# Kernel tuning notes

Measured on AMD Instinct MI355X. Metric: run time of the kernel, lower is better.

Reference implementation:

```python
import jax, jax.numpy as jnp
import numpy as np

B, M, N, HID, H, P = 16, 1024, 1024, 512, 8, 2
DH = HID // H


def setup_inputs() -> dict:
    key = jax.random.key(0)
    k1, k2, k3, k4 = jax.random.split(key, 4)
    X = jax.random.normal(k1, (B, M, HID), dtype=jnp.float32)
    Y = jax.random.normal(k2, (B, N, HID), dtype=jnp.float32)
    # learned pad prefixes (kaiming-uniform in torch; any init is fine for a numerics baseline)
    bound = np.sqrt(1.0 / HID)
    pad_x = jax.random.uniform(k3, (P, HID), dtype=jnp.float32, minval=-bound, maxval=bound)
    pad_y = jax.random.uniform(k4, (P, HID), dtype=jnp.float32, minval=-bound, maxval=bound)
    return {"X": X, "Y": Y, "pad_x": pad_x, "pad_y": pad_y}


def _project(T, pad):
    # prepend learned pad rows, split into heads -> [B, H, L+P, DH]
    b = T.shape[0]
    T = jnp.concatenate([jnp.broadcast_to(pad[None], (b, P, HID)), T], axis=1)
    return T.reshape(b, T.shape[1], H, DH).transpose(0, 2, 1, 3)


def reference(X, Y, pad_x, pad_y):
    Xp = _project(X, pad_x)  # [B,H,Mp,DH], query=key=value
    Yp = _project(Y, pad_y)  # [B,H,Np,DH]
    # shared similarity matrix (no 1/sqrt(d) scaling in the original)
    sim = jnp.einsum('bhmd,bhnd->bhmn', Xp, Yp)  # [B,H,Mp,Np]
    # masks in the original are all-ones (pad rows + torch.ones), so masked_fill is a no-op
    attn_X_by_Y = jax.nn.softmax(sim, axis=2)  # softmax over Mp (rows)
    attn_Y_by_X = jax.nn.softmax(sim, axis=3)  # softmax over Np (cols)
    # X attends in Y: attn^T @ X_value -> [B,H,Np,DH]
    X_in_Y = jnp.einsum('bhmn,bhmd->bhnd', attn_X_by_Y, Xp)[:, :, P:, :]
    X_in_Y = X_in_Y.transpose(0, 2, 1, 3).reshape(X.shape[0], -1, HID)  # [B,N,HID]
    # Y attends in X: attn @ Y_value -> [B,H,Mp,DH]
    Y_in_X = jnp.einsum('bhmn,bhnd->bhmd', attn_Y_by_X, Yp)[:, :, P:, :]
    Y_in_X = Y_in_X.transpose(0, 2, 1, 3).reshape(Y.shape[0], -1, HID)  # [B,M,HID]
    return X_in_Y, Y_in_X
```

## Files before the change

kernel.cpp:

```cpp
#include <hip/hip_runtime.h>
#include <hip/hip_bf16.h>
#include <stdint.h>

typedef _Float16 f16x8_t __attribute__((ext_vector_type(8)));
typedef _Float16 f16x2_t __attribute__((ext_vector_type(2)));
typedef float    f32x4_t __attribute__((ext_vector_type(4)));
typedef short    s16x8_t __attribute__((ext_vector_type(8)));
typedef unsigned int u32;

#define MFMA16 __builtin_amdgcn_mfma_f32_16x16x32_f16

#if __has_builtin(__builtin_amdgcn_exp2f)
#define EXP2(x) __builtin_amdgcn_exp2f(x)
#else
#define EXP2(x) exp2f(x)
#endif

__device__ __forceinline__ u32 PKRTZ(float a, float b) {
    return __builtin_bit_cast(u32, __builtin_amdgcn_cvt_pkrtz(a, b));
}

constexpr int Bb   = 16;
constexpr int HIDc = 512;
constexpr int DHc  = 64;
constexpr int SEQc = 1024;

constexpr int QT = 128;
constexpr int KT = 64;
constexpr int NTILES = SEQc / KT;

constexpr float LOG2E_F = 1.4426950408889634f;
constexpr float DTHR    = 11.5f;

constexpr int ROWB    = 144;
constexpr int K_BASE  = 0;
constexpr int VT_BASE = 64 * ROWB;
constexpr int P_BASE  = VT_BASE + 80 * ROWB;
constexpr int P_WAVE  = 16 * ROWB;
constexpr int LDS_TOTAL = P_BASE + 4 * P_WAVE;

__global__ __launch_bounds__(256, 4)
void xattn_kernel(const float* __restrict__ X, const float* __restrict__ Y,
                  const float* __restrict__ padx, const float* __restrict__ pady,
                  float* __restrict__ out)
{
    __shared__ __align__(16) unsigned char pool[LDS_TOTAL];

    const int tid  = threadIdx.x;
    const int w    = tid >> 6;
    const int lane = tid & 63;
    const int g    = lane >> 4;
    const int q16  = lane & 15;

    const unsigned hid = blockIdx.x + gridDim.x * (blockIdx.y + gridDim.y * blockIdx.z);
    const unsigned lid = (hid & 7u) * 256u + (hid >> 3);
    const int qt   = lid & 7;
    const int bh   = (lid >> 3) & 127;
    const int pass = lid >> 10;
    const int b    = bh >> 3;
    const int h    = bh & 7;

    const float* Qp   = pass == 0 ? X : Y;
    const float* KVp  = pass == 0 ? Y : X;
    const float* padp = pass == 0 ? pady : padx;
    float* outp = out + (pass == 0 ? (size_t)Bb * SEQc * HIDc : (size_t)0);

    f16x8_t qf[2][2];
#pragma unroll
    for (int sub = 0; sub < 2; ++sub) {
        const float* qrow = Qp + ((size_t)b * SEQc + qt * QT + w * 32 + sub * 16 + q16) * HIDc + h * DHc;
#pragma unroll
        for (int s = 0; s < 2; ++s) {
            const float* src = qrow + s * 32 + g * 8;
            float4 a = *(const float4*)src;
            float4 c = *(const float4*)(src + 4);
            u32 p0 = PKRTZ(a.x * LOG2E_F, a.y * LOG2E_F);
            u32 p1 = PKRTZ(a.z * LOG2E_F, a.w * LOG2E_F);
            u32 p2 = PKRTZ(c.x * LOG2E_F, c.y * LOG2E_F);
            u32 p3 = PKRTZ(c.z * LOG2E_F, c.w * LOG2E_F);
            uint4 uu = {p0, p1, p2, p3};
            qf[sub][s] = __builtin_bit_cast(f16x8_t, uu);
        }
    }

    const float* padh = padp + h * DHc;
    float m0r, m1r;
    f32x4_t Oacc0[4], Oacc1[4], lext0, lext1;
    {
#pragma unroll
        for (int sub = 0; sub < 2; ++sub) {
            float s0 = 0.f, s1 = 0.f;
#pragma unroll
            for (int s = 0; s < 2; ++s)
#pragma unroll
                for (int j = 0; j < 8; ++j) {
                    float qv = (float)qf[sub][s][j];
                    int d = s * 32 + g * 8 + j;
                    s0 += qv * padh[d];
                    s1 += qv * padh[HIDc + d];
                }
            s0 += __shfl_xor(s0, 16); s0 += __shfl_xor(s0, 32);
            s1 += __shfl_xor(s1, 16); s1 += __shfl_xor(s1, 32);
            float m = fmaxf(s0, s1);
            float e0 = EXP2(s0 - m), e1 = EXP2(s1 - m);
            f32x4_t* Oa = sub ? Oacc1 : Oacc0;
#pragma unroll
            for (int db = 0; db < 4; ++db)
#pragma unroll
                for (int i = 0; i < 4; ++i) {
                    int d = db * 16 + g * 4 + i;
                    Oa[db][i] = e0 * padh[d] + e1 * padh[HIDc + d];
                }
            f32x4_t le = {0.f, 0.f, 0.f, 0.f};
            le[0] = (g == 0) ? (e0 + e1) : 0.f;
            if (sub) { lext1 = le; m1r = m; } else { lext0 = le; m0r = m; }
        }
    }

    unsigned vaddr[2][5];
#pragma unroll
    for (int t = 0; t < 2; ++t)
#pragma unroll
        for (int db = 0; db < 5; ++db) {
            int row = db * 16 + q16;
            int sw  = (db * 2 + (q16 >> 3)) & 7;
            vaddr[t][db] = (unsigned)(VT_BASE + row * ROWB + (((t * 4 + g) ^ sw) << 4));
        }
    const unsigned kb0 = (unsigned)(K_BASE + q16 * ROWB + g * 16);
    const unsigned pwb = (unsigned)(P_BASE + w * P_WAVE + q16 * ROWB + g * 8);
    const unsigned prb = (unsigned)(P_BASE + w * P_WAVE + q16 * ROWB + g * 16);

    const int tr = tid >> 3, tc = tid & 7;
    const float* ksrc = KVp + ((size_t)b * SEQc + 2 * tr) * HIDc + h * DHc + tc * 8;
    const unsigned kwb  = (unsigned)(K_BASE + (2 * tr) * ROWB + tc * 16);
    const unsigned vtwb = (unsigned)(VT_BASE + (tc * 8) * ROWB + (((tr >> 2) ^ tc) << 4) + (tr & 3) * 4);

#pragma unroll
    for (int it = 0; it < 2; ++it) {
        int idx = tid + it * 256;
        int row = 64 + (idx >> 5);
        int wd  = idx & 31;
        u32 val = (row == 64) ? 0x3C003C00u : 0u;
        unsigned a = (unsigned)(VT_BASE + row * ROWB + (((wd >> 2) ^ ((row >> 3) & 7)) << 4) + (wd & 3) * 4);
        *(u32*)(pool + a) = val;
    }

    auto softmax_pv = [&](f32x4_t (&sacc)[4], f32x4_t (&Oacc)[4], f32x4_t& lext, float& mrun) {
        float pmax = fmaxf(fmaxf(fmaxf(sacc[0][0], sacc[0][1]), fmaxf(sacc[0][2], sacc[0][3])),
                           fmaxf(fmaxf(sacc[1][0], sacc[1][1]), fmaxf(sacc[1][2], sacc[1][3])));
        float pmax2 = fmaxf(fmaxf(fmaxf(sacc[2][0], sacc[2][1]), fmaxf(sacc[2][2], sacc[2][3])),
                            fmaxf(fmaxf(sacc[3][0], sacc[3][1]), fmaxf(sacc[3][2], sacc[3][3])));
        pmax = fmaxf(pmax, pmax2);
        pmax = fmaxf(pmax, __shfl_xor(pmax, 16));
        pmax = fmaxf(pmax, __shfl_xor(pmax, 32));
        if (!__all(pmax <= mrun + DTHR)) {
            float mnew = fmaxf(mrun, pmax);
            float corr = EXP2(mrun - mnew);
            mrun = mnew;
#pragma unroll
            for (int db = 0; db < 4; ++db)
#pragma unroll
                for (int i = 0; i < 4; ++i) Oacc[db][i] *= corr;
            lext[0] *= corr;
        }
        const float m = mrun;
#pragma unroll
        for (int nb = 0; nb < 4; ++nb) {
            u32 w0 = PKRTZ(EXP2(sacc[nb][0] - m), EXP2(sacc[nb][1] - m));
            u32 w1 = PKRTZ(EXP2(sacc[nb][2] - m), EXP2(sacc[nb][3] - m));
            uint2 pk = {w0, w1};
            *(uint2*)(pool + pwb + nb * 32) = pk;
        }
        asm volatile("" ::: "memory");
#pragma unroll
        for (int t = 0; t < 2; ++t) {
            f16x8_t pb = __builtin_bit_cast(f16x8_t, *(const s16x8_t*)(pool + prb + t * 64));
#pragma unroll
            for (int db = 0; db < 4; ++db) {
                s16x8_t va = *(const s16x8_t*)(pool + vaddr[t][db]);
                Oacc[db] = MFMA16(__builtin_bit_cast(f16x8_t, va), pb, Oacc[db], 0, 0, 0);
            }
            s16x8_t v1 = *(const s16x8_t*)(pool + vaddr[t][4]);
            lext = MFMA16(__builtin_bit_cast(f16x8_t, v1), pb, lext, 0, 0, 0);
        }
    };

    for (int kt = 0; kt < NTILES; ++kt) {
        __syncthreads();
        {
            const float* srow = ksrc + (size_t)kt * KT * HIDc;
            float4 a0 = *(const float4*)srow;
            float4 a1 = *(const float4*)(srow + 4);
            float4 c0 = *(const float4*)(srow + HIDc);
            float4 c1 = *(const float4*)(srow + HIDc + 4);
            uint4 k0 = {PKRTZ(a0.x, a0.y), PKRTZ(a0.z, a0.w), PKRTZ(a1.x, a1.y), PKRTZ(a1.z, a1.w)};
            uint4 k1 = {PKRTZ(c0.x, c0.y), PKRTZ(c0.z, c0.w), PKRTZ(c1.x, c1.y), PKRTZ(c1.z, c1.w)};
            *(uint4*)(pool + kwb) = k0;
            *(uint4*)(pool + kwb + ROWB) = k1;
            float fa[8] = {a0.x, a0.y, a0.z, a0.w, a1.x, a1.y, a1.z, a1.w};
            float fc[8] = {c0.x, c0.y, c0.z, c0.w, c1.x, c1.y, c1.z, c1.w};
#pragma unroll
            for (int j = 0; j < 8; ++j)
                *(u32*)(pool + vtwb + j * ROWB) = PKRTZ(fa[j], fc[j]);
        }
        __syncthreads();

        f32x4_t sacc0[4], sacc1[4];
#pragma unroll
        for (int nb = 0; nb < 4; ++nb) {
            sacc0[nb] = f32x4_t{0.f, 0.f, 0.f, 0.f};
            sacc1[nb] = f32x4_t{0.f, 0.f, 0.f, 0.f};
        }
#pragma unroll
        for (int s = 0; s < 2; ++s)
#pragma unroll
            for (int nb = 0; nb < 4; ++nb) {
                s16x8_t kh = *(const s16x8_t*)(pool + kb0 + nb * (16 * ROWB) + s * 64);
                f16x8_t kf = __builtin_bit_cast(f16x8_t, kh);
                sacc0[nb] = MFMA16(kf, qf[0][s], sacc0[nb], 0, 0, 0);
                sacc1[nb] = MFMA16(kf, qf[1][s], sacc1[nb], 0, 0, 0);
            }

        softmax_pv(sacc0, Oacc0, lext0, m0r);
        softmax_pv(sacc1, Oacc1, lext1, m1r);
    }

    float lv0 = __shfl(lext0[0], q16);
    float lv1 = __shfl(lext1[0], q16);
    const float inv[2] = {1.0f / lv0, 1.0f / lv1};
    float* fp = (float*)pool;
    const int r = tid >> 2, c = tid & 3;
#pragma unroll
    for (int sub = 0; sub < 2; ++sub) {
        __syncthreads();
        const f32x4_t* Oa = sub ? Oacc1 : Oacc0;
#pragma unroll
        for (int db = 0; db < 4; ++db)
#pragma unroll
            for (int i = 0; i < 4; ++i)
                fp[(w * 16 + q16) * 68 + db * 16 + g * 4 + i] = Oa[db][i] * inv[sub];
        __syncthreads();
        const int grow = qt * QT + (r >> 4) * 32 + sub * 16 + (r & 15);
        float* dst = outp + ((size_t)b * SEQc + grow) * HIDc + h * DHc + c * 16;
        const float* srcp = fp + r * 68 + c * 16;
#pragma unroll
        for (int k = 0; k < 4; ++k)
            *(float4*)(dst + k * 4) = *(const float4*)(srcp + k * 4);
    }
}

extern "C" void kernel_launch(void* const* d_in, const int* in_sizes, int n_in,
                              void* d_out, int out_size, void* d_ws, size_t ws_size,
                              hipStream_t stream) {
    const float* X    = (const float*)d_in[0];
    const float* Y    = (const float*)d_in[1];
    const float* padx = (const float*)d_in[2];
    const float* pady = (const float*)d_in[3];
    float* out = (float*)d_out;
    (void)in_sizes; (void)n_in; (void)out_size; (void)d_ws; (void)ws_size;

    dim3 grid(SEQc / QT, Bb * 8, 2);
    hipLaunchKernelGGL(xattn_kernel, grid, dim3(256), 0, stream, X, Y, padx, pady, out);
}
```

Baseline: 121.6 us.

## Prefetch next K/V tile into registers and raise wave priority around MFMAs

```diff
diff --git a/kernel.cpp b/kernel.cpp
--- a/kernel.cpp
+++ b/kernel.cpp
@@ -3,7 +3,6 @@
 #include <stdint.h>
 
 typedef _Float16 f16x8_t __attribute__((ext_vector_type(8)));
-typedef _Float16 f16x2_t __attribute__((ext_vector_type(2)));
 typedef float    f32x4_t __attribute__((ext_vector_type(4)));
 typedef short    s16x8_t __attribute__((ext_vector_type(8)));
 typedef unsigned int u32;
@@ -172,6 +171,7 @@
             *(uint2*)(pool + pwb + nb * 32) = pk;
         }
         asm volatile("" ::: "memory");
+        __builtin_amdgcn_s_setprio(1);
 #pragma unroll
         for (int t = 0; t < 2; ++t) {
             f16x8_t pb = __builtin_bit_cast(f16x8_t, *(const s16x8_t*)(pool + prb + t * 64));
@@ -183,34 +183,17 @@
             s16x8_t v1 = *(const s16x8_t*)(pool + vaddr[t][4]);
             lext = MFMA16(__builtin_bit_cast(f16x8_t, v1), pb, lext, 0, 0, 0);
         }
+        __builtin_amdgcn_s_setprio(0);
     };
 
-    for (int kt = 0; kt < NTILES; ++kt) {
-        __syncthreads();
-        {
-            const float* srow = ksrc + (size_t)kt * KT * HIDc;
-            float4 a0 = *(const float4*)srow;
-            float4 a1 = *(const float4*)(srow + 4);
-            float4 c0 = *(const float4*)(srow + HIDc);
-            float4 c1 = *(const float4*)(srow + HIDc + 4);
-            uint4 k0 = {PKRTZ(a0.x, a0.y), PKRTZ(a0.z, a0.w), PKRTZ(a1.x, a1.y), PKRTZ(a1.z, a1.w)};
-            uint4 k1 = {PKRTZ(c0.x, c0.y), PKRTZ(c0.z, c0.w), PKRTZ(c1.x, c1.y), PKRTZ(c1.z, c1.w)};
-            *(uint4*)(pool + kwb) = k0;
-            *(uint4*)(pool + kwb + ROWB) = k1;
-            float fa[8] = {a0.x, a0.y, a0.z, a0.w, a1.x, a1.y, a1.z, a1.w};
-            float fc[8] = {c0.x, c0.y, c0.z, c0.w, c1.x, c1.y, c1.z, c1.w};
-#pragma unroll
-            for (int j = 0; j < 8; ++j)
-                *(u32*)(pool + vtwb + j * ROWB) = PKRTZ(fa[j], fc[j]);
-        }
-        __syncthreads();
-
+    auto compute_tile = [&]() {
         f32x4_t sacc0[4], sacc1[4];
 #pragma unroll
         for (int nb = 0; nb < 4; ++nb) {
             sacc0[nb] = f32x4_t{0.f, 0.f, 0.f, 0.f};
             sacc1[nb] = f32x4_t{0.f, 0.f, 0.f, 0.f};
         }
+        __builtin_amdgcn_s_setprio(1);
 #pragma unroll
         for (int s = 0; s < 2; ++s)
 #pragma unroll
@@ -220,10 +203,45 @@
                 sacc0[nb] = MFMA16(kf, qf[0][s], sacc0[nb], 0, 0, 0);
                 sacc1[nb] = MFMA16(kf, qf[1][s], sacc1[nb], 0, 0, 0);
             }
-
+        __builtin_amdgcn_s_setprio(0);
         softmax_pv(sacc0, Oacc0, lext0, m0r);
         softmax_pv(sacc1, Oacc1, lext1, m1r);
-    }
+    };
+
+    float4 Aa0, Aa1, Ac0, Ac1, Ba0, Ba1, Bc0, Bc1;
+#define LOADSET(r0, r1, r2, r3, idx)  {                                        \
+        const float* srow_ = ksrc + (size_t)(idx) * KT * HIDc;                 \
+        r0 = *(const float4*)srow_;          r1 = *(const float4*)(srow_ + 4); \
+        r2 = *(const float4*)(srow_ + HIDc); r3 = *(const float4*)(srow_ + HIDc + 4); }
+#define STAGESET(a0, a1, c0, c1) {                                             \
+        uint4 k0 = {PKRTZ(a0.x, a0.y), PKRTZ(a0.z, a0.w), PKRTZ(a1.x, a1.y), PKRTZ(a1.z, a1.w)}; \
+        uint4 k1 = {PKRTZ(c0.x, c0.y), PKRTZ(c0.z, c0.w), PKRTZ(c1.x, c1.y), PKRTZ(c1.z, c1.w)}; \
+        *(uint4*)(pool + kwb) = k0;                                            \
+        *(uint4*)(pool + kwb + ROWB) = k1;                                     \
+        float fa_[8] = {a0.x, a0.y, a0.z, a0.w, a1.x, a1.y, a1.z, a1.w};       \
+        float fc_[8] = {c0.x, c0.y, c0.z, c0.w, c1.x, c1.y, c1.z, c1.w};       \
+        _Pragma("unroll")                                                      \
+        for (int j_ = 0; j_ < 8; ++j_)                                         \
+            *(u32*)(pool + vtwb + j_ * ROWB) = PKRTZ(fa_[j_], fc_[j_]); }
+
+    LOADSET(Aa0, Aa1, Ac0, Ac1, 0);
+    for (int kt = 0; kt < NTILES; kt += 2) {
+        __syncthreads();
+        STAGESET(Aa0, Aa1, Ac0, Ac1);
+        LOADSET(Ba0, Ba1, Bc0, Bc1, kt + 1);
+        __syncthreads();
+        compute_tile();
+        __syncthreads();
+        STAGESET(Ba0, Ba1, Bc0, Bc1);
+        {
+            int nxt = kt + 2 < NTILES ? kt + 2 : NTILES - 1;
+            LOADSET(Aa0, Aa1, Ac0, Ac1, nxt);
+        }
+        __syncthreads();
+        compute_tile();
+    }
+#undef LOADSET
+#undef STAGESET
 
     float lv0 = __shfl(lext0[0], q16);
     float lv1 = __shfl(lext1[0], q16);
```

Result: slower. 148.7 us (+22.4%).
